# Kernel optimization log

Hardware: AMD Instinct MI355X
Metric: run time of the kernel (lower is better)

The kernel has to match this reference:

```python
import jax, jax.numpy as jnp
import numpy as np
import math

D_MODEL = 256
D_STATE = 16
D_CONV = 4
EXPAND = 2
D_INNER = EXPAND * D_MODEL          # 512
DT_RANK = math.ceil(D_MODEL / 16)   # 16
EPS = 1e-5


def rmsnorm(x, w):
    return x * jax.lax.rsqrt(jnp.mean(x * x, axis=-1, keepdims=True) + EPS) * w


def mamba_mixer(x, in_proj, conv_w, conv_b, x_proj, dt_w, dt_b, A_log, Dp, out_proj):
    # x: [B, L, d_model]
    Bsz, L, _ = x.shape
    xz = x @ in_proj.T                       # [B, L, 2*d_inner]
    xh, z = jnp.split(xz, 2, axis=-1)        # each [B, L, d_inner]
    # causal depthwise conv1d over time (d_conv=4)
    xp = jnp.pad(xh, ((0, 0), (D_CONV - 1, 0), (0, 0)))
    xc = sum(xp[:, k:k + L, :] * conv_w[:, k] for k in range(D_CONV)) + conv_b
    xc = jax.nn.silu(xc)                     # [B, L, d_inner]
    x_dbl = xc @ x_proj.T                    # [B, L, dt_rank + 2*d_state]
    dt, Bm, Cm = jnp.split(x_dbl, [DT_RANK, DT_RANK + D_STATE], axis=-1)
    delta = jax.nn.softplus(dt @ dt_w.T + dt_b)   # [B, L, d_inner]
    A = -jnp.exp(A_log)                      # [d_inner, d_state]
    dA = jnp.exp(jnp.einsum('bld,dn->lbdn', delta, A))        # [L,B,d,n]
    dBu = jnp.einsum('bld,bln,bld->lbdn', delta, Bm, xc)       # [L,B,d,n]

    def step(h, inp):
        a, b = inp
        h = a * h + b
        return h, h

    h0 = jnp.zeros((Bsz, D_INNER, D_STATE), xc.dtype)
    _, hs = jax.lax.scan(step, h0, (dA, dBu))                  # [L,B,d,n]
    y = jnp.einsum('lbdn,bln->bld', hs, Cm) + xc * Dp          # [B,L,d_inner]
    y = y * jax.nn.silu(z)
    return y @ out_proj.T                                      # [B,L,d_model]


def block(x, norm_w, in_proj, conv_w, conv_b, x_proj, dt_w, dt_b, A_log, Dp, out_proj):
    # Block with fused_add_norm=False, residual=None: residual = x, h = mixer(norm(x))
    residual = x
    h = mamba_mixer(rmsnorm(x, norm_w), in_proj, conv_w, conv_b, x_proj,
                    dt_w, dt_b, A_log, Dp, out_proj)
    return h + residual


def setup_inputs() -> dict:
    key = jax.random.key(0)
    ks = jax.random.split(key, 16)
    B, L = 4, 2048

    def n(k, shape, s=0.02):
        return jax.random.normal(k, shape, jnp.float32) * s

    inp = {"x": jax.random.normal(ks[0], (B, L, D_MODEL), jnp.float32)}
    i = 1
    for pre in ("fw", "bw"):
        inp[pre + "_norm"] = jnp.ones((D_MODEL,), jnp.float32)
        inp[pre + "_in_proj"] = n(ks[i], (2 * D_INNER, D_MODEL)); i += 1
        inp[pre + "_conv_w"] = n(ks[i], (D_INNER, D_CONV), 0.1); i += 1
        inp[pre + "_conv_b"] = jnp.zeros((D_INNER,), jnp.float32)
        inp[pre + "_x_proj"] = n(ks[i], (DT_RANK + 2 * D_STATE, D_INNER)); i += 1
        inp[pre + "_dt_w"] = n(ks[i], (D_INNER, DT_RANK), 0.1); i += 1
        inp[pre + "_dt_b"] = n(ks[i], (D_INNER,), 0.1); i += 1
        inp[pre + "_A_log"] = jnp.log(jnp.tile(jnp.arange(1, D_STATE + 1, dtype=jnp.float32), (D_INNER, 1)))
        inp[pre + "_D"] = jnp.ones((D_INNER,), jnp.float32)
        inp[pre + "_out_proj"] = n(ks[i], (D_MODEL, D_INNER)); i += 1
    return inp


def reference(x,
              fw_norm, fw_in_proj, fw_conv_w, fw_conv_b, fw_x_proj, fw_dt_w, fw_dt_b, fw_A_log, fw_D, fw_out_proj,
              bw_norm, bw_in_proj, bw_conv_w, bw_conv_b, bw_x_proj, bw_dt_w, bw_dt_b, bw_A_log, bw_D, bw_out_proj):
    fwd = block(x, fw_norm, fw_in_proj, fw_conv_w, fw_conv_b, fw_x_proj,
                fw_dt_w, fw_dt_b, fw_A_log, fw_D, fw_out_proj)
    xb = jnp.flip(x, axis=1)
    bwd = block(xb, bw_norm, bw_in_proj, bw_conv_w, bw_conv_b, bw_x_proj,
                bw_dt_w, bw_dt_b, bw_A_log, bw_D, bw_out_proj)
    bwd = jnp.flip(bwd, axis=1)
    return fwd + bwd
```

## Files before the change

### kernel.cpp

```cpp
#include <hip/hip_runtime.h>
#include <hip/hip_bf16.h>
#include <math.h>


#define NTOK 8192
#define LL   2048
#define DM   256
#define DI   512
#define DS2  16
#define CL   64
#define NCH  32
#define PLANE 65536
#define KSTEP 64

typedef __bf16 bf16x8 __attribute__((ext_vector_type(8)));
typedef float f32x4 __attribute__((ext_vector_type(4)));

__device__ inline unsigned short f2bf(float f) {
    unsigned u = __float_as_uint(f);
    unsigned r = (u + 0x7fffu + ((u >> 16) & 1u)) >> 16;
    return (unsigned short)r;
}
__device__ inline float bf2f(unsigned short s) {
    return __uint_as_float((unsigned)s << 16);
}

#define L2E 1.4426950408889634f
#define LN2 0.6931471805599453f

__device__ inline float softplus_fast(float x) {
    float e = __builtin_amdgcn_exp2f(-fabsf(x) * L2E);
    float l = __builtin_amdgcn_logf(1.f + e);
    return fmaxf(x, 0.f) + l * LN2;
}

__device__ inline int xcd_swz(int bid, int nwg) {
    int q = nwg >> 3, r = nwg & 7;
    int xcd = bid & 7, lo = bid >> 3;
    return (xcd < r ? xcd * (q + 1) : r * (q + 1) + (xcd - r) * q) + lo;
}

#define GLDS(gp, lp) __builtin_amdgcn_global_load_lds( \
    (const __attribute__((address_space(1))) void*)(gp), \
    (__attribute__((address_space(3))) void*)(lp), 16, 0, 0)

__global__ __launch_bounds__(256) void prep_kernel(
    const float* __restrict__ ip0, const float* __restrict__ nw0,
    const float* __restrict__ ip1, const float* __restrict__ nw1,
    const float* __restrict__ xp0, const float* __restrict__ dtw0,
    const float* __restrict__ xp1, const float* __restrict__ dtw1,
    const float* __restrict__ op0, const float* __restrict__ op1,
    unsigned short* __restrict__ w_in, unsigned short* __restrict__ w_p2,
    unsigned short* __restrict__ w_out,
    const float* __restrict__ x, unsigned short* __restrict__ xn) {
    int bid = blockIdx.x, tid = threadIdx.x;
    if (bid < 2048) {
        int dir = bid >> 10, n = bid & 1023;
        const float* ip = dir ? ip1 : ip0;
        const float* nw = dir ? nw1 : nw0;
        w_in[(size_t)bid * 256 + tid] = f2bf(ip[n * 256 + tid] * nw[tid]);
    } else if (bid < 3200) {
        int idx = bid - 2048;
        int dir = idx / 576, row = idx % 576;
        const float* xp = dir ? xp1 : xp0;
        const float* dtw = dir ? dtw1 : dtw0;
        unsigned short* dst = w_p2 + (size_t)idx * 512;
        for (int k = tid; k < 512; k += 256) {
            float v = 0.f;
            if (row < 512) {
                #pragma unroll
                for (int r = 0; r < 16; ++r) v = fmaf(dtw[row * 16 + r], xp[r * 512 + k], v);
            } else if (row < 544) {
                v = xp[(16 + row - 512) * 512 + k];
            }
            dst[k] = f2bf(v);
        }
    } else if (bid < 3456) {
        int n = bid - 3200;
        for (int k = tid; k < 1024; k += 256) {
            float v = (k < 512) ? op0[n * 512 + k] : op1[n * 512 + (k - 512)];
            w_out[(size_t)n * 1024 + k] = f2bf(v);
        }
    } else {
        int t = bid - 3456;
        float v = x[(size_t)t * DM + tid];
        float ss = v * v;
        #pragma unroll
        for (int m = 1; m < 64; m <<= 1) ss += __shfl_xor(ss, m);
        __shared__ float ws[4];
        if ((tid & 63) == 0) ws[tid >> 6] = ss;
        __syncthreads();
        float tot = ws[0] + ws[1] + ws[2] + ws[3];
        float scale = rsqrtf(tot / (float)DM + 1e-5f);
        xn[(size_t)t * DM + tid] = f2bf(v * scale);
    }
}

#define EPI_IN  0
#define EPI_P2  1
#define EPI_OUT 2

template <int EPI>
__global__ __launch_bounds__(256) void mfma_gemm(
    const unsigned short* __restrict__ A0, const unsigned short* __restrict__ A1,
    const unsigned short* __restrict__ Wb, int K,
    unsigned short* __restrict__ d0, unsigned short* __restrict__ d1,
    unsigned short* __restrict__ e0, unsigned short* __restrict__ e1,
    const float* __restrict__ aux0, const float* __restrict__ aux1,
    const float* __restrict__ Xres, float* __restrict__ outF) {
    __shared__ char lds[2][2][8192];
    int tid = threadIdx.x;
    int lane = tid & 63, wid = tid >> 6;
    int wm = wid >> 1, wn = wid & 1;
    int nwg = gridDim.x * gridDim.y;
    int lid = xcd_swz(blockIdx.y * gridDim.x + blockIdx.x, nwg);
    int n0 = (lid % gridDim.x) * 64;
    int m0 = (lid / gridDim.x) * 64;
    int dir = blockIdx.z;
    const unsigned short* A = dir ? A1 : A0;
    const unsigned short* W = Wb + ((EPI == EPI_P2) ? (size_t)dir * 576 * 512 : 0);

    const int s1 = tid, s2 = tid + 256;
    const int r1 = s1 >> 3, c1 = (s1 & 7) ^ (r1 & 7);
    const int r2 = s2 >> 3, c2 = (s2 & 7) ^ (r2 & 7);

    f32x4 acc[2][2] = {};
    int nt = K / KSTEP;

    auto stage = [&](int t, int buf) {
        int k0 = t * KSTEP;
        GLDS(A + (size_t)(m0 + r1) * K + k0 + c1 * 8, &lds[buf][0][0] + wid * 1024);
        GLDS(A + (size_t)(m0 + r2) * K + k0 + c2 * 8, &lds[buf][0][0] + 4096 + wid * 1024);
        GLDS(W + (size_t)(n0 + r1) * K + k0 + c1 * 8, &lds[buf][1][0] + wid * 1024);
        GLDS(W + (size_t)(n0 + r2) * K + k0 + c2 * 8, &lds[buf][1][0] + 4096 + wid * 1024);
    };

    stage(0, 0);
    for (int t = 0; t < nt; ++t) {
        int buf = t & 1;
        __syncthreads();
        if (t + 1 < nt) stage(t + 1, buf ^ 1);
        const char* Ab = &lds[buf][0][0];
        const char* Bb = &lds[buf][1][0];
        bf16x8 af[2][2], bfv[2][2];
        #pragma unroll
        for (int mf = 0; mf < 2; ++mf)
            #pragma unroll
            for (int kf = 0; kf < 2; ++kf) {
                int r = wm * 32 + mf * 16 + (lane & 15);
                int c = (lane >> 4) + kf * 4;
                af[mf][kf] = *(const bf16x8*)(Ab + r * 128 + ((c ^ (r & 7)) << 4));
            }
        #pragma unroll
        for (int nf = 0; nf < 2; ++nf)
            #pragma unroll
            for (int kf = 0; kf < 2; ++kf) {
                int r = wn * 32 + nf * 16 + (lane & 15);
                int c = (lane >> 4) + kf * 4;
                bfv[nf][kf] = *(const bf16x8*)(Bb + r * 128 + ((c ^ (r & 7)) << 4));
            }
        #pragma unroll
        for (int kf = 0; kf < 2; ++kf)
            #pragma unroll
            for (int mf = 0; mf < 2; ++mf)
                #pragma unroll
                for (int nf = 0; nf < 2; ++nf)
                    acc[mf][nf] = __builtin_amdgcn_mfma_f32_16x16x32_bf16(
                        af[mf][kf], bfv[nf][kf], acc[mf][nf], 0, 0, 0);
    }

    int cb0 = n0 + wn * 32 + (lane & 15);
    int rb0 = m0 + wm * 32 + ((lane >> 4) << 2);
    #pragma unroll
    for (int mf = 0; mf < 2; ++mf)
        #pragma unroll
        for (int nf = 0; nf < 2; ++nf) {
            int n = cb0 + nf * 16;
            #pragma unroll
            for (int r = 0; r < 4; ++r) {
                int m = rb0 + mf * 16 + r;
                float v = acc[mf][nf][r];
                if (EPI == EPI_IN) {
                    d0[(size_t)m * 2048 + n] = f2bf(v);
                } else if (EPI == EPI_P2) {
                    if (n < 512) {
                        float sv = v + (dir ? aux1 : aux0)[n];
                        (dir ? d1 : d0)[(size_t)m * 512 + n] = f2bf(softplus_fast(sv));
                    } else if (n < 544) {
                        (dir ? e1 : e0)[(size_t)m * 32 + (n - 512)] = f2bf(v);
                    }
                } else {
                    outF[(size_t)m * 256 + n] = v + 2.f * Xres[(size_t)m * 256 + n];
                }
            }
        }
}

__global__ __launch_bounds__(256) void conv_silu_kernel(
    const unsigned short* __restrict__ xz,
    const float* __restrict__ cw0, const float* __restrict__ cw1,
    const float* __restrict__ cb0, const float* __restrict__ cb1,
    unsigned short* __restrict__ o0, unsigned short* __restrict__ o1) {
    int dir = blockIdx.y;
    const float* cw = dir ? cw1 : cw0;
    const float* cb = dir ? cb1 : cb0;
    unsigned short* xc = dir ? o1 : o0;
    int idx8 = blockIdx.x * 256 + threadIdx.x;
    int t = idx8 >> 6;
    int c8 = (idx8 & 63) << 3;
    int l = t & (LL - 1);
    const unsigned short* xh = xz + (size_t)dir * 1024 + c8;

    float wreg[32];
    #pragma unroll
    for (int q = 0; q < 8; ++q)
        *(float4*)&wreg[q * 4] = *(const float4*)&cw[c8 * 4 + q * 4];
    float acc[8];
    *(float4*)&acc[0] = *(const float4*)&cb[c8];
    *(float4*)&acc[4] = *(const float4*)&cb[c8 + 4];

    #pragma unroll
    for (int k = 0; k < 4; ++k) {
        int lo = dir ? (l + 3 - k) : (l - 3 + k);
        if (lo < 0 || lo >= LL) continue;
        uint4 u = *(const uint4*)(xh + (size_t)(t + lo - l) * 2048);
        unsigned wv[4] = {u.x, u.y, u.z, u.w};
        #pragma unroll
        for (int j = 0; j < 4; ++j) {
            float flo = __uint_as_float(wv[j] << 16);
            float fhi = __uint_as_float(wv[j] & 0xffff0000u);
            acc[2 * j]     = fmaf(flo, wreg[(2 * j) * 4 + k], acc[2 * j]);
            acc[2 * j + 1] = fmaf(fhi, wreg[(2 * j + 1) * 4 + k], acc[2 * j + 1]);
        }
    }
    unsigned out[4];
    #pragma unroll
    for (int j = 0; j < 4; ++j) {
        float a0 = acc[2 * j], a1 = acc[2 * j + 1];
        float s0 = a0 / (1.f + __expf(-a0));
        float s1 = a1 / (1.f + __expf(-a1));
        out[j] = (unsigned)f2bf(s0) | ((unsigned)f2bf(s1) << 16);
    }
    *(uint4*)(xc + (size_t)idx8 * 8) = make_uint4(out[0], out[1], out[2], out[3]);
}

__global__ __launch_bounds__(256, 4) void scan_part1(
    const unsigned short* __restrict__ dlt0, const unsigned short* __restrict__ dlt1,
    const unsigned short* __restrict__ xc0, const unsigned short* __restrict__ xc1,
    const unsigned short* __restrict__ bc0, const unsigned short* __restrict__ bc1,
    const float* __restrict__ Al0, const float* __restrict__ Al1,
    const float* __restrict__ Dp0, const float* __restrict__ Dp1,
    float* __restrict__ AC, float* __restrict__ HC,
    unsigned* __restrict__ yls0, unsigned* __restrict__ yls1) {
    int dir = blockIdx.z;
    const unsigned short* delta = dir ? dlt1 : dlt0;
    const unsigned short* xc    = dir ? xc1 : xc0;
    const unsigned short* bc    = dir ? bc1 : bc0;
    const float* Alog           = dir ? Al1 : Al0;
    const float* Dp             = dir ? Dp1 : Dp0;
    unsigned* yls               = dir ? yls1 : yls0;
    int b = blockIdx.y >> 5, ch = blockIdx.y & 31;
    int d0 = blockIdx.x * 128;
    int tid = threadIdx.x;
    int dg = tid >> 1, nq = tid & 1;
    int d = d0 + dg;

    __shared__ unsigned sdxu[CL][128];
    __shared__ unsigned sBC[CL][16];
    {
        int row = tid >> 2, q = tid & 3;
        int lr = ch * CL + row;
        int l = dir ? (LL - 1 - lr) : lr;
        size_t t = (size_t)b * LL + l;
        const uint4* dp = (const uint4*)(delta + t * DI + d0 + q * 32);
        const uint4* xp = (const uint4*)(xc + t * DI + d0 + q * 32);
        #pragma unroll
        for (int hh = 0; hh < 4; ++hh) {
            uint4 du = dp[hh], xu = xp[hh];
            unsigned dw[4] = {du.x, du.y, du.z, du.w};
            unsigned xw[4] = {xu.x, xu.y, xu.z, xu.w};
            #pragma unroll
            for (int j = 0; j < 4; ++j) {
                int col = q * 32 + hh * 8 + 2 * j;
                sdxu[row][col ^ row]       = (dw[j] & 0xffffu) | (xw[j] << 16);
                sdxu[row][(col + 1) ^ row] = (dw[j] >> 16) | (xw[j] & 0xffff0000u);
            }
        }
        uint2 Bu = *(const uint2*)(bc + t * 32 + q * 4);
        uint2 Cu = *(const uint2*)(bc + t * 32 + 16 + q * 4);
        sBC[row][q * 4 + 0] = (Bu.x & 0xffffu) | (Cu.x << 16);
        sBC[row][q * 4 + 1] = (Bu.x >> 16) | (Cu.x & 0xffff0000u);
        sBC[row][q * 4 + 2] = (Bu.y & 0xffffu) | (Cu.y << 16);
        sBC[row][q * 4 + 3] = (Bu.y >> 16) | (Cu.y & 0xffff0000u);
    }
    __syncthreads();

    float Av[8], Avl[8];
    {
        float4 Ala = *(const float4*)&Alog[d * DS2 + nq * 8];
        float4 Alb = *(const float4*)&Alog[d * DS2 + nq * 8 + 4];
        Av[0] = -__expf(Ala.x); Av[1] = -__expf(Ala.y);
        Av[2] = -__expf(Ala.z); Av[3] = -__expf(Ala.w);
        Av[4] = -__expf(Alb.x); Av[5] = -__expf(Alb.y);
        Av[6] = -__expf(Alb.z); Av[7] = -__expf(Alb.w);
    }
    #pragma unroll
    for (int j = 0; j < 8; ++j) Avl[j] = Av[j] * L2E;
    bool fast = true;
    #pragma unroll
    for (int j = 0; j < 7; ++j)
        fast = fast && (fabsf(Av[j + 1] - Av[j] + 1.f) < 1e-2f);

    float Dv = Dp[d];
    float h[8] = {0.f, 0.f, 0.f, 0.f, 0.f, 0.f, 0.f, 0.f};
    float sdl = 0.f;
    const float nL2E = -L2E;

    if (fast) {
        #pragma unroll 2
        for (int r = 0; r < CL; ++r) {
            unsigned u = sdxu[r][dg ^ r];
            float dl = __uint_as_float(u << 16);
            float xcv = __uint_as_float(u & 0xffff0000u);
            uint4 q0 = *(const uint4*)&sBC[r][nq * 8];
            uint4 q1 = *(const uint4*)&sBC[r][nq * 8 + 4];
            unsigned bw[8] = {q0.x, q0.y, q0.z, q0.w, q1.x, q1.y, q1.z, q1.w};
            float u0 = dl * xcv;
            sdl += dl;
            float e  = __builtin_amdgcn_exp2f(dl * Avl[0]);
            float rr = __builtin_amdgcn_exp2f(dl * nL2E);
            float ts = 0.f;
            #pragma unroll
            for (int j = 0; j < 8; ++j) {
                float Bf = __uint_as_float(bw[j] << 16);
                float Cf = __uint_as_float(bw[j] & 0xffff0000u);
                h[j] = fmaf(e, h[j], u0 * Bf);
                ts = fmaf(h[j], Cf, ts);
                if (j < 7) e *= rr;
            }
            ts += __shfl_xor(ts, 1);
            if (nq == 0) {
                int lr = ch * CL + r;
                float yv = fmaf(xcv, Dv, ts);
                yls[((size_t)b * LL + lr) * DI + d] =
                    (unsigned)f2bf(yv) | ((unsigned)f2bf(sdl) << 16);
            }
        }
    } else {
        #pragma unroll 2
        for (int r = 0; r < CL; ++r) {
            unsigned u = sdxu[r][dg ^ r];
            float dl = __uint_as_float(u << 16);
            float xcv = __uint_as_float(u & 0xffff0000u);
            uint4 q0 = *(const uint4*)&sBC[r][nq * 8];
            uint4 q1 = *(const uint4*)&sBC[r][nq * 8 + 4];
            unsigned bw[8] = {q0.x, q0.y, q0.z, q0.w, q1.x, q1.y, q1.z, q1.w};
            float u0 = dl * xcv;
            sdl += dl;
            float ts = 0.f;
            #pragma unroll
            for (int j = 0; j < 8; ++j) {
                float Bf = __uint_as_float(bw[j] << 16);
                float Cf = __uint_as_float(bw[j] & 0xffff0000u);
                float e = __builtin_amdgcn_exp2f(dl * Avl[j]);
                h[j] = fmaf(e, h[j], u0 * Bf);
                ts = fmaf(h[j], Cf, ts);
            }
            ts += __shfl_xor(ts, 1);
            if (nq == 0) {
                int lr = ch * CL + r;
                float yv = fmaf(xcv, Dv, ts);
                yls[((size_t)b * LL + lr) * DI + d] =
                    (unsigned)f2bf(yv) | ((unsigned)f2bf(sdl) << 16);
            }
        }
    }

    size_t base = (size_t)ch * PLANE + (size_t)(((dir * 4 + b) * DI + d) * DS2 + nq * 8);
    float ac[8];
    #pragma unroll
    for (int j = 0; j < 8; ++j) ac[j] = __builtin_amdgcn_exp2f(Avl[j] * sdl);
    *(float4*)&AC[base]     = make_float4(ac[0], ac[1], ac[2], ac[3]);
    *(float4*)&AC[base + 4] = make_float4(ac[4], ac[5], ac[6], ac[7]);
    *(float4*)&HC[base]     = make_float4(h[0], h[1], h[2], h[3]);
    *(float4*)&HC[base + 4] = make_float4(h[4], h[5], h[6], h[7]);
}

__global__ __launch_bounds__(256) void scan_part2(
    const float* __restrict__ AC, const float* __restrict__ HC,
    float* __restrict__ HIN) {
    int idx = blockIdx.x * 256 + threadIdx.x;
    float hin = 0.f;
    #pragma unroll
    for (int ch = 0; ch < NCH; ++ch) {
        size_t o = (size_t)ch * PLANE + idx;
        HIN[o] = hin;
        hin = fmaf(AC[o], hin, HC[o]);
    }
}

__global__ __launch_bounds__(256, 8) void scan_lite(
    const unsigned* __restrict__ yls0, const unsigned* __restrict__ yls1,
    const unsigned short* __restrict__ bc0, const unsigned short* __restrict__ bc1,
    const unsigned short* __restrict__ xz,
    const float* __restrict__ Al0, const float* __restrict__ Al1,
    const float* __restrict__ HIN, unsigned short* __restrict__ ycat) {
    int dir = blockIdx.z;
    const unsigned* yls         = dir ? yls1 : yls0;
    const unsigned short* bc    = dir ? bc1 : bc0;
    const float* Alog           = dir ? Al1 : Al0;
    int b = blockIdx.y >> 5, ch = blockIdx.y & 31;
    int d0 = blockIdx.x * 64;
    int tid = threadIdx.x;
    int dg = tid & 63, lg = tid >> 6;
    int d = d0 + dg;

    __shared__ unsigned sC[CL][8];
    {
        int row = tid >> 2, q = tid & 3;
        if (q < 2) {
            int lr = ch * CL + row;
            int l = dir ? (LL - 1 - lr) : lr;
            size_t t = (size_t)b * LL + l;
            uint4 cu = *(const uint4*)(bc + t * 32 + 16 + q * 8);
            *(uint4*)&sC[row][q * 4] = cu;
        }
    }
    __syncthreads();

    float Av[16];
    bool fastA = true;
    #pragma unroll
    for (int qq = 0; qq < 4; ++qq) {
        float4 Al = *(const float4*)&Alog[d * DS2 + qq * 4];
        Av[qq * 4 + 0] = -__expf(Al.x);
        Av[qq * 4 + 1] = -__expf(Al.y);
        Av[qq * 4 + 2] = -__expf(Al.z);
        Av[qq * 4 + 3] = -__expf(Al.w);
    }
    #pragma unroll
    for (int n = 0; n < 16; ++n)
        fastA = fastA && (fabsf(Av[n] + (float)(n + 1)) < 1e-3f * (float)(n + 1));

    float hin[16];
    size_t hbase = (size_t)ch * PLANE + (size_t)(((dir * 4 + b) * DI + d) * DS2);
    #pragma unroll
    for (int qq = 0; qq < 4; ++qq)
        *(float4*)&hin[qq * 4] = *(const float4*)&HIN[hbase + qq * 4];

    #pragma unroll 2
    for (int i = 0; i < 16; ++i) {
        int row = lg * 16 + i;
        int lr = ch * CL + row;
        int ll = dir ? (LL - 1 - lr) : lr;
        size_t tt = (size_t)b * LL + ll;
        unsigned u = yls[((size_t)b * LL + lr) * DI + d];
        float yv = __uint_as_float(u << 16);
        float s  = __uint_as_float(u & 0xffff0000u);
        if (fastA) {
            float E = __builtin_amdgcn_exp2f(-s * L2E);
            if (__any(E > 3e-6f)) {
                float acc = 0.f;
                #pragma unroll
                for (int p = 7; p >= 0; --p) {
                    unsigned cp = sC[row][p];
                    float C0 = __uint_as_float(cp << 16);
                    float C1 = __uint_as_float(cp & 0xffff0000u);
                    acc = fmaf(acc, E, C1 * hin[2 * p + 1]);
                    acc = fmaf(acc, E, C0 * hin[2 * p]);
                }
                yv = fmaf(acc, E, yv);
            }
        } else {
            float acc = 0.f;
            #pragma unroll
            for (int p = 0; p < 8; ++p) {
                unsigned cp = sC[row][p];
                float C0 = __uint_as_float(cp << 16);
                float C1 = __uint_as_float(cp & 0xffff0000u);
                float e0 = __builtin_amdgcn_exp2f(s * Av[2 * p] * L2E);
                float e1 = __builtin_amdgcn_exp2f(s * Av[2 * p + 1] * L2E);
                acc = fmaf(e0 * hin[2 * p], C0, acc);
                acc = fmaf(e1 * hin[2 * p + 1], C1, acc);
            }
            yv += acc;
        }
        float zz = bf2f(xz[tt * 2048 + (size_t)dir * 1024 + 512 + d]);
        yv *= zz / (1.f + __expf(-zz));
        ycat[tt * 1024 + (size_t)dir * 512 + d] = f2bf(yv);
    }
}

extern "C" void kernel_launch(void* const* d_in, const int* in_sizes, int n_in,
                              void* d_out, int out_size, void* d_ws, size_t ws_size,
                              hipStream_t stream) {
    const float* x = (const float*)d_in[0];
    const float* p[2][10];
    for (int dir = 0; dir < 2; ++dir)
        for (int i = 0; i < 10; ++i)
            p[dir][i] = (const float*)d_in[1 + dir * 10 + i];

    char* w = (char*)d_ws;
    auto alloc = [&](size_t bytes) { char* q = w; w += (bytes + 255) & ~(size_t)255; return q; };
    unsigned short* xn    = (unsigned short*)alloc((size_t)NTOK * DM * 2);
    unsigned short* w_in  = (unsigned short*)alloc((size_t)2048 * 256 * 2);
    unsigned short* w_p2  = (unsigned short*)alloc((size_t)1152 * 512 * 2);
    unsigned short* w_out = (unsigned short*)alloc((size_t)256 * 1024 * 2);
    unsigned short* xzcat = (unsigned short*)alloc((size_t)NTOK * 2048 * 2);
    unsigned short *xcb[2], *dlt[2], *bc[2];
    unsigned* yls[2];
    for (int dir = 0; dir < 2; ++dir) {
        xcb[dir] = (unsigned short*)alloc((size_t)NTOK * DI * 2);
        dlt[dir] = (unsigned short*)alloc((size_t)NTOK * DI * 2);
        bc[dir]  = (unsigned short*)alloc((size_t)NTOK * 32 * 2);
        yls[dir] = (unsigned*)alloc((size_t)NTOK * DI * 4);
    }
    unsigned short* ycat = (unsigned short*)alloc((size_t)NTOK * 1024 * 2);
    float* AC  = (float*)alloc((size_t)NCH * PLANE * 4);
    float* HC  = (float*)alloc((size_t)NCH * PLANE * 4);
    float* HIN = (float*)alloc((size_t)NCH * PLANE * 4);
    float* out = (float*)d_out;

    prep_kernel<<<3456 + NTOK, 256, 0, stream>>>(
        p[0][1], p[0][0], p[1][1], p[1][0],
        p[0][4], p[0][5], p[1][4], p[1][5],
        p[0][9], p[1][9], w_in, w_p2, w_out, x, xn);

    mfma_gemm<EPI_IN><<<dim3(32, 128, 1), 256, 0, stream>>>(
        xn, xn, w_in, 256, xzcat, nullptr, nullptr, nullptr,
        nullptr, nullptr, nullptr, nullptr);

    conv_silu_kernel<<<dim3(2048, 2), 256, 0, stream>>>(
        xzcat, p[0][2], p[1][2], p[0][3], p[1][3], xcb[0], xcb[1]);

    mfma_gemm<EPI_P2><<<dim3(9, 128, 2), 256, 0, stream>>>(
        xcb[0], xcb[1], w_p2, 512, dlt[0], dlt[1], bc[0], bc[1],
        p[0][6], p[1][6], nullptr, nullptr);

    scan_part1<<<dim3(DI / 128, 4 * NCH, 2), 256, 0, stream>>>(
        dlt[0], dlt[1], xcb[0], xcb[1], bc[0], bc[1], p[0][7], p[1][7],
        p[0][8], p[1][8], AC, HC, yls[0], yls[1]);
    scan_part2<<<PLANE / 256, 256, 0, stream>>>(AC, HC, HIN);
    scan_lite<<<dim3(DI / 64, 4 * NCH, 2), 256, 0, stream>>>(
        yls[0], yls[1], bc[0], bc[1], xzcat,
        p[0][7], p[1][7], HIN, ycat);

    mfma_gemm<EPI_OUT><<<dim3(4, 128, 1), 256, 0, stream>>>(
        ycat, ycat, w_out, 1024, nullptr, nullptr, nullptr, nullptr,
        nullptr, nullptr, x, out);
}
```

Before: 169.9 us.

## Halve scan_part1 shared staging, transpose yls layout, and break exp dependency chain

scan_part1 now stages the delta/xc chunk in two 32-row halves, which halves the sdxu shared buffer, and raises the launch-bounds occupancy hint from 4 to 8 blocks. The intermediate yls buffer is transposed to a [b][d][l] layout so each thread writes four timesteps in one 16-byte store and scan_part3 reads 16 consecutive values with vector loads. In the fast path, the sequential e*=rr chain is replaced with a power tree, and the C dot product is split into two accumulators to shorten the dependency chains. The cost is an extra pair of barriers, with half the threads idle while each half is staged, and more register pressure under the tighter launch bound.

New measurement: 187.8 us. +10.5%, slower.

```diff
diff --git a/kernel.cpp b/kernel.cpp
--- a/kernel.cpp
+++ b/kernel.cpp
@@ -244,7 +244,7 @@
     *(uint4*)(xc + (size_t)idx8 * 8) = make_uint4(out[0], out[1], out[2], out[3]);
 }
 
-__global__ __launch_bounds__(256, 4) void scan_part1(
+__global__ __launch_bounds__(256, 8) void scan_part1(
     const unsigned short* __restrict__ dlt0, const unsigned short* __restrict__ dlt1,
     const unsigned short* __restrict__ xc0, const unsigned short* __restrict__ xc1,
     const unsigned short* __restrict__ bc0, const unsigned short* __restrict__ bc1,
@@ -265,34 +265,48 @@
     int dg = tid >> 1, nq = tid & 1;
     int d = d0 + dg;
 
-    __shared__ unsigned sdxu[CL][128];
+    __shared__ unsigned sdxu[32][128];
     __shared__ unsigned sBC[CL][16];
-    {
-        int row = tid >> 2, q = tid & 3;
-        int lr = ch * CL + row;
-        int l = dir ? (LL - 1 - lr) : lr;
-        size_t t = (size_t)b * LL + l;
-        const uint4* dp = (const uint4*)(delta + t * DI + d0 + q * 32);
-        const uint4* xp = (const uint4*)(xc + t * DI + d0 + q * 32);
-        #pragma unroll
-        for (int hh = 0; hh < 4; ++hh) {
-            uint4 du = dp[hh], xu = xp[hh];
-            unsigned dw[4] = {du.x, du.y, du.z, du.w};
-            unsigned xw[4] = {xu.x, xu.y, xu.z, xu.w};
-            #pragma unroll
-            for (int j = 0; j < 4; ++j) {
-                int col = q * 32 + hh * 8 + 2 * j;
-                sdxu[row][col ^ row]       = (dw[j] & 0xffffu) | (xw[j] << 16);
-                sdxu[row][(col + 1) ^ row] = (dw[j] >> 16) | (xw[j] & 0xffff0000u);
-            }
-        }
-        uint2 Bu = *(const uint2*)(bc + t * 32 + q * 4);
-        uint2 Cu = *(const uint2*)(bc + t * 32 + 16 + q * 4);
-        sBC[row][q * 4 + 0] = (Bu.x & 0xffffu) | (Cu.x << 16);
-        sBC[row][q * 4 + 1] = (Bu.x >> 16) | (Cu.x & 0xffff0000u);
-        sBC[row][q * 4 + 2] = (Bu.y & 0xffffu) | (Cu.y << 16);
-        sBC[row][q * 4 + 3] = (Bu.y >> 16) | (Cu.y & 0xffff0000u);
-    }
+
+    auto stage_half = [&](int h) {
+        if (tid < 128) {
+            int row = tid >> 2, q = tid & 3;
+            int lr = ch * CL + h * 32 + row;
+            int l = dir ? (LL - 1 - lr) : lr;
+            size_t t = (size_t)b * LL + l;
+            const uint4* dp = (const uint4*)(delta + t * DI + d0);
+            const uint4* xp = (const uint4*)(xc + t * DI + d0);
+            #pragma unroll
+            for (int hh = 0; hh < 4; ++hh) {
+                uint4 du = dp[hh * 4 + q], xu = xp[hh * 4 + q];
+                unsigned dw[4] = {du.x, du.y, du.z, du.w};
+                unsigned xw[4] = {xu.x, xu.y, xu.z, xu.w};
+                #pragma unroll
+                for (int j = 0; j < 4; ++j) {
+                    int col = hh * 32 + q * 8 + 2 * j;
+                    sdxu[row][col ^ row]       = (dw[j] & 0xffffu) | (xw[j] << 16);
+                    sdxu[row][(col + 1) ^ row] = (dw[j] >> 16) | (xw[j] & 0xffff0000u);
+                }
+            }
+        } else if (h == 0) {
+            int tid2 = tid - 128;
+            int row = tid2 >> 1, qh = tid2 & 1;
+            int lr = ch * CL + row;
+            int l = dir ? (LL - 1 - lr) : lr;
+            size_t t = (size_t)b * LL + l;
+            #pragma unroll
+            for (int qi = 0; qi < 2; ++qi) {
+                int q = qh * 2 + qi;
+                uint2 Bu = *(const uint2*)(bc + t * 32 + q * 4);
+                uint2 Cu = *(const uint2*)(bc + t * 32 + 16 + q * 4);
+                *(uint4*)&sBC[row][q * 4] = make_uint4(
+                    (Bu.x & 0xffffu) | (Cu.x << 16), (Bu.x >> 16) | (Cu.x & 0xffff0000u),
+                    (Bu.y & 0xffffu) | (Cu.y << 16), (Bu.y >> 16) | (Cu.y & 0xffff0000u));
+            }
+        }
+    };
+
+    stage_half(0);
     __syncthreads();
 
     float Av[8], Avl[8];
@@ -315,63 +329,79 @@
     float h[8] = {0.f, 0.f, 0.f, 0.f, 0.f, 0.f, 0.f, 0.f};
     float sdl = 0.f;
     const float nL2E = -L2E;
-
-    if (fast) {
-        #pragma unroll 2
-        for (int r = 0; r < CL; ++r) {
-            unsigned u = sdxu[r][dg ^ r];
-            float dl = __uint_as_float(u << 16);
-            float xcv = __uint_as_float(u & 0xffff0000u);
-            uint4 q0 = *(const uint4*)&sBC[r][nq * 8];
-            uint4 q1 = *(const uint4*)&sBC[r][nq * 8 + 4];
-            unsigned bw[8] = {q0.x, q0.y, q0.z, q0.w, q1.x, q1.y, q1.z, q1.w};
-            float u0 = dl * xcv;
-            sdl += dl;
-            float e  = __builtin_amdgcn_exp2f(dl * Avl[0]);
-            float rr = __builtin_amdgcn_exp2f(dl * nL2E);
-            float ts = 0.f;
-            #pragma unroll
-            for (int j = 0; j < 8; ++j) {
-                float Bf = __uint_as_float(bw[j] << 16);
-                float Cf = __uint_as_float(bw[j] & 0xffff0000u);
-                h[j] = fmaf(e, h[j], u0 * Bf);
-                ts = fmaf(h[j], Cf, ts);
-                if (j < 7) e *= rr;
-            }
-            ts += __shfl_xor(ts, 1);
-            if (nq == 0) {
-                int lr = ch * CL + r;
-                float yv = fmaf(xcv, Dv, ts);
-                yls[((size_t)b * LL + lr) * DI + d] =
-                    (unsigned)f2bf(yv) | ((unsigned)f2bf(sdl) << 16);
-            }
-        }
-    } else {
-        #pragma unroll 2
-        for (int r = 0; r < CL; ++r) {
-            unsigned u = sdxu[r][dg ^ r];
-            float dl = __uint_as_float(u << 16);
-            float xcv = __uint_as_float(u & 0xffff0000u);
-            uint4 q0 = *(const uint4*)&sBC[r][nq * 8];
-            uint4 q1 = *(const uint4*)&sBC[r][nq * 8 + 4];
-            unsigned bw[8] = {q0.x, q0.y, q0.z, q0.w, q1.x, q1.y, q1.z, q1.w};
-            float u0 = dl * xcv;
-            sdl += dl;
-            float ts = 0.f;
-            #pragma unroll
-            for (int j = 0; j < 8; ++j) {
-                float Bf = __uint_as_float(bw[j] << 16);
-                float Cf = __uint_as_float(bw[j] & 0xffff0000u);
-                float e = __builtin_amdgcn_exp2f(dl * Avl[j]);
-                h[j] = fmaf(e, h[j], u0 * Bf);
-                ts = fmaf(h[j], Cf, ts);
-            }
-            ts += __shfl_xor(ts, 1);
-            if (nq == 0) {
-                int lr = ch * CL + r;
-                float yv = fmaf(xcv, Dv, ts);
-                yls[((size_t)b * LL + lr) * DI + d] =
-                    (unsigned)f2bf(yv) | ((unsigned)f2bf(sdl) << 16);
+    unsigned ybuf[4];
+    size_t ybase = ((size_t)b * DI + d) * LL + (size_t)ch * CL;
+
+    for (int half = 0; half < 2; ++half) {
+        if (half) { __syncthreads(); stage_half(1); __syncthreads(); }
+        if (fast) {
+            #pragma unroll 2
+            for (int rl = 0; rl < 32; ++rl) {
+                int r = half * 32 + rl;
+                unsigned u = sdxu[rl][dg ^ rl];
+                float dl = __uint_as_float(u << 16);
+                float xcv = __uint_as_float(u & 0xffff0000u);
+                uint4 q0 = *(const uint4*)&sBC[r][nq * 8];
+                uint4 q1 = *(const uint4*)&sBC[r][nq * 8 + 4];
+                unsigned bw[8] = {q0.x, q0.y, q0.z, q0.w, q1.x, q1.y, q1.z, q1.w};
+                float u0 = dl * xcv;
+                sdl += dl;
+                float e0 = __builtin_amdgcn_exp2f(dl * Avl[0]);
+                float rr = __builtin_amdgcn_exp2f(dl * nL2E);
+                float rr2 = rr * rr, rr4 = rr2 * rr2;
+                float e[8];
+                e[0] = e0;         e[1] = e0 * rr;
+                e[2] = e0 * rr2;   e[3] = e[1] * rr2;
+                e[4] = e0 * rr4;   e[5] = e[1] * rr4;
+                e[6] = e[2] * rr4; e[7] = e[3] * rr4;
+                float tsa = 0.f, tsb = 0.f;
+                #pragma unroll
+                for (int j = 0; j < 8; ++j) {
+                    float Bf = __uint_as_float(bw[j] << 16);
+                    float Cf = __uint_as_float(bw[j] & 0xffff0000u);
+                    h[j] = fmaf(e[j], h[j], u0 * Bf);
+                    if (j & 1) tsb = fmaf(h[j], Cf, tsb);
+                    else       tsa = fmaf(h[j], Cf, tsa);
+                }
+                float ts = tsa + tsb;
+                ts += __shfl_xor(ts, 1);
+                if (nq == 0) {
+                    float yv = fmaf(xcv, Dv, ts);
+                    ybuf[r & 3] = (unsigned)f2bf(yv) | ((unsigned)f2bf(sdl) << 16);
+                    if ((r & 3) == 3)
+                        *(uint4*)&yls[ybase + (r - 3)] =
+                            make_uint4(ybuf[0], ybuf[1], ybuf[2], ybuf[3]);
+                }
+            }
+        } else {
+            #pragma unroll 2
+            for (int rl = 0; rl < 32; ++rl) {
+                int r = half * 32 + rl;
+                unsigned u = sdxu[rl][dg ^ rl];
+                float dl = __uint_as_float(u << 16);
+                float xcv = __uint_as_float(u & 0xffff0000u);
+                uint4 q0 = *(const uint4*)&sBC[r][nq * 8];
+                uint4 q1 = *(const uint4*)&sBC[r][nq * 8 + 4];
+                unsigned bw[8] = {q0.x, q0.y, q0.z, q0.w, q1.x, q1.y, q1.z, q1.w};
+                float u0 = dl * xcv;
+                sdl += dl;
+                float ts = 0.f;
+                #pragma unroll
+                for (int j = 0; j < 8; ++j) {
+                    float Bf = __uint_as_float(bw[j] << 16);
+                    float Cf = __uint_as_float(bw[j] & 0xffff0000u);
+                    float e = __builtin_amdgcn_exp2f(dl * Avl[j]);
+                    h[j] = fmaf(e, h[j], u0 * Bf);
+                    ts = fmaf(h[j], Cf, ts);
+                }
+                ts += __shfl_xor(ts, 1);
+                if (nq == 0) {
+                    float yv = fmaf(xcv, Dv, ts);
+                    ybuf[r & 3] = (unsigned)f2bf(yv) | ((unsigned)f2bf(sdl) << 16);
+                    if ((r & 3) == 3)
+                        *(uint4*)&yls[ybase + (r - 3)] =
+                            make_uint4(ybuf[0], ybuf[1], ybuf[2], ybuf[3]);
+                }
             }
         }
     }
@@ -448,13 +478,19 @@
     for (int qq = 0; qq < 4; ++qq)
         *(float4*)&hin[qq * 4] = *(const float4*)&HIN[hbase + qq * 4];
 
+    unsigned yv4[16];
+    const unsigned* yp = &yls[((size_t)b * DI + d) * LL + (size_t)ch * CL + lg * 16];
+    #pragma unroll
+    for (int k = 0; k < 4; ++k)
+        *(uint4*)&yv4[k * 4] = *(const uint4*)(yp + k * 4);
+
     #pragma unroll 2
     for (int i = 0; i < 16; ++i) {
         int row = lg * 16 + i;
         int lr = ch * CL + row;
         int ll = dir ? (LL - 1 - lr) : lr;
         size_t tt = (size_t)b * LL + ll;
-        unsigned u = yls[((size_t)b * LL + lr) * DI + d];
+        unsigned u = yv4[i];
         float yv = __uint_as_float(u << 16);
         float s  = __uint_as_float(u & 0xffff0000u);
         if (fastA) {
```

## Halve scan chunk length, double chunk count, and shorten per-step decay chain

Applied to the files above, without the earlier changes.

Cuts the chunked selective-scan chunk length from 64 to 32 and doubles the chunk count, remapping the shared-memory staging loads in scan_part1 and scan_lite and raising scan_part1's occupancy hint to 8. This gives more concurrent blocks and a shorter serial recurrence per block. Inside the fast path, the per-state decay factors are now computed as a shallow tree of powers instead of a serial multiply chain, and the C-dot product uses two accumulators to add instruction-level parallelism. The cost is more chunk-boundary state traffic through AC/HC/HIN and a longer serial loop in scan_part2.

Result: no change. 171.4 us (+0.9%).

```diff
diff --git a/kernel.cpp b/kernel.cpp
--- a/kernel.cpp
+++ b/kernel.cpp
@@ -8,8 +8,8 @@
 #define DM   256
 #define DI   512
 #define DS2  16
-#define CL   64
-#define NCH  32
+#define CL   32
+#define NCH  64
 #define PLANE 65536
 #define KSTEP 64
 
@@ -244,7 +244,7 @@
     *(uint4*)(xc + (size_t)idx8 * 8) = make_uint4(out[0], out[1], out[2], out[3]);
 }
 
-__global__ __launch_bounds__(256, 4) void scan_part1(
+__global__ __launch_bounds__(256, 8) void scan_part1(
     const unsigned short* __restrict__ dlt0, const unsigned short* __restrict__ dlt1,
     const unsigned short* __restrict__ xc0, const unsigned short* __restrict__ xc1,
     const unsigned short* __restrict__ bc0, const unsigned short* __restrict__ bc1,
@@ -259,7 +259,7 @@
     const float* Alog           = dir ? Al1 : Al0;
     const float* Dp             = dir ? Dp1 : Dp0;
     unsigned* yls               = dir ? yls1 : yls0;
-    int b = blockIdx.y >> 5, ch = blockIdx.y & 31;
+    int b = blockIdx.y >> 6, ch = blockIdx.y & 63;
     int d0 = blockIdx.x * 128;
     int tid = threadIdx.x;
     int dg = tid >> 1, nq = tid & 1;
@@ -268,30 +268,31 @@
     __shared__ unsigned sdxu[CL][128];
     __shared__ unsigned sBC[CL][16];
     {
-        int row = tid >> 2, q = tid & 3;
+        int row = tid >> 3, q = tid & 7;
         int lr = ch * CL + row;
         int l = dir ? (LL - 1 - lr) : lr;
         size_t t = (size_t)b * LL + l;
-        const uint4* dp = (const uint4*)(delta + t * DI + d0 + q * 32);
-        const uint4* xp = (const uint4*)(xc + t * DI + d0 + q * 32);
-        #pragma unroll
-        for (int hh = 0; hh < 4; ++hh) {
-            uint4 du = dp[hh], xu = xp[hh];
+        const uint4* dp = (const uint4*)(delta + t * DI + d0);
+        const uint4* xp = (const uint4*)(xc + t * DI + d0);
+        #pragma unroll
+        for (int hh = 0; hh < 2; ++hh) {
+            uint4 du = dp[q * 2 + hh], xu = xp[q * 2 + hh];
             unsigned dw[4] = {du.x, du.y, du.z, du.w};
             unsigned xw[4] = {xu.x, xu.y, xu.z, xu.w};
             #pragma unroll
             for (int j = 0; j < 4; ++j) {
-                int col = q * 32 + hh * 8 + 2 * j;
+                int col = q * 16 + hh * 8 + 2 * j;
                 sdxu[row][col ^ row]       = (dw[j] & 0xffffu) | (xw[j] << 16);
                 sdxu[row][(col + 1) ^ row] = (dw[j] >> 16) | (xw[j] & 0xffff0000u);
             }
         }
-        uint2 Bu = *(const uint2*)(bc + t * 32 + q * 4);
-        uint2 Cu = *(const uint2*)(bc + t * 32 + 16 + q * 4);
-        sBC[row][q * 4 + 0] = (Bu.x & 0xffffu) | (Cu.x << 16);
-        sBC[row][q * 4 + 1] = (Bu.x >> 16) | (Cu.x & 0xffff0000u);
-        sBC[row][q * 4 + 2] = (Bu.y & 0xffffu) | (Cu.y << 16);
-        sBC[row][q * 4 + 3] = (Bu.y >> 16) | (Cu.y & 0xffff0000u);
+        if (q < 4) {
+            uint2 Bu = *(const uint2*)(bc + t * 32 + q * 4);
+            uint2 Cu = *(const uint2*)(bc + t * 32 + 16 + q * 4);
+            *(uint4*)&sBC[row][q * 4] = make_uint4(
+                (Bu.x & 0xffffu) | (Cu.x << 16), (Bu.x >> 16) | (Cu.x & 0xffff0000u),
+                (Bu.y & 0xffffu) | (Cu.y << 16), (Bu.y >> 16) | (Cu.y & 0xffff0000u));
+        }
     }
     __syncthreads();
 
@@ -327,17 +328,24 @@
             unsigned bw[8] = {q0.x, q0.y, q0.z, q0.w, q1.x, q1.y, q1.z, q1.w};
             float u0 = dl * xcv;
             sdl += dl;
-            float e  = __builtin_amdgcn_exp2f(dl * Avl[0]);
+            float e0 = __builtin_amdgcn_exp2f(dl * Avl[0]);
             float rr = __builtin_amdgcn_exp2f(dl * nL2E);
-            float ts = 0.f;
+            float rr2 = rr * rr, rr4 = rr2 * rr2;
+            float e[8];
+            e[0] = e0;         e[1] = e0 * rr;
+            e[2] = e0 * rr2;   e[3] = e[1] * rr2;
+            e[4] = e0 * rr4;   e[5] = e[1] * rr4;
+            e[6] = e[2] * rr4; e[7] = e[3] * rr4;
+            float tsa = 0.f, tsb = 0.f;
             #pragma unroll
             for (int j = 0; j < 8; ++j) {
                 float Bf = __uint_as_float(bw[j] << 16);
                 float Cf = __uint_as_float(bw[j] & 0xffff0000u);
-                h[j] = fmaf(e, h[j], u0 * Bf);
-                ts = fmaf(h[j], Cf, ts);
-                if (j < 7) e *= rr;
-            }
+                h[j] = fmaf(e[j], h[j], u0 * Bf);
+                if (j & 1) tsb = fmaf(h[j], Cf, tsb);
+                else       tsa = fmaf(h[j], Cf, tsa);
+            }
+            float ts = tsa + tsb;
             ts += __shfl_xor(ts, 1);
             if (nq == 0) {
                 int lr = ch * CL + r;
@@ -391,7 +399,7 @@
     float* __restrict__ HIN) {
     int idx = blockIdx.x * 256 + threadIdx.x;
     float hin = 0.f;
-    #pragma unroll
+    #pragma unroll 8
     for (int ch = 0; ch < NCH; ++ch) {
         size_t o = (size_t)ch * PLANE + idx;
         HIN[o] = hin;
@@ -409,22 +417,20 @@
     const unsigned* yls         = dir ? yls1 : yls0;
     const unsigned short* bc    = dir ? bc1 : bc0;
     const float* Alog           = dir ? Al1 : Al0;
-    int b = blockIdx.y >> 5, ch = blockIdx.y & 31;
+    int b = blockIdx.y >> 6, ch = blockIdx.y & 63;
     int d0 = blockIdx.x * 64;
     int tid = threadIdx.x;
     int dg = tid & 63, lg = tid >> 6;
     int d = d0 + dg;
 
     __shared__ unsigned sC[CL][8];
-    {
-        int row = tid >> 2, q = tid & 3;
-        if (q < 2) {
-            int lr = ch * CL + row;
-            int l = dir ? (LL - 1 - lr) : lr;
-            size_t t = (size_t)b * LL + l;
-            uint4 cu = *(const uint4*)(bc + t * 32 + 16 + q * 8);
-            *(uint4*)&sC[row][q * 4] = cu;
-        }
+    if (tid < 64) {
+        int row = tid >> 1, q = tid & 1;
+        int lr = ch * CL + row;
+        int l = dir ? (LL - 1 - lr) : lr;
+        size_t t = (size_t)b * LL + l;
+        uint4 cu = *(const uint4*)(bc + t * 32 + 16 + q * 8);
+        *(uint4*)&sC[row][q * 4] = cu;
     }
     __syncthreads();
 
@@ -449,8 +455,8 @@
         *(float4*)&hin[qq * 4] = *(const float4*)&HIN[hbase + qq * 4];
 
     #pragma unroll 2
-    for (int i = 0; i < 16; ++i) {
-        int row = lg * 16 + i;
+    for (int i = 0; i < 8; ++i) {
+        int row = lg * 8 + i;
         int lr = ch * CL + row;
         int ll = dir ? (LL - 1 - lr) : lr;
         size_t tt = (size_t)b * LL + ll;
```

## Assign one channel per thread with all 16 states in scan_part1

Applied to the files above, without the earlier changes.

scan_part1 now runs 128 threads per block, each owning a single d channel and all 16 state entries, where before two threads split the 16 states and combined results with a shuffle. B and C are stored in shared memory already converted to float, the decay powers come from a power-of-two tree instead of a serial multiply chain, and the C dot product uses four partial accumulators. This removes the cross-lane shuffle and halves the redundant delta/x work per channel, at the cost of more registers per thread and half as many threads per block, which lowers occupancy and latency hiding.

Result: no change. 168.6 us (-0.8%).

```diff
diff --git a/kernel.cpp b/kernel.cpp
--- a/kernel.cpp
+++ b/kernel.cpp
@@ -244,7 +244,7 @@
     *(uint4*)(xc + (size_t)idx8 * 8) = make_uint4(out[0], out[1], out[2], out[3]);
 }
 
-__global__ __launch_bounds__(256, 4) void scan_part1(
+__global__ __launch_bounds__(128, 2) void scan_part1(
     const unsigned short* __restrict__ dlt0, const unsigned short* __restrict__ dlt1,
     const unsigned short* __restrict__ xc0, const unsigned short* __restrict__ xc1,
     const unsigned short* __restrict__ bc0, const unsigned short* __restrict__ bc1,
@@ -262,128 +262,138 @@
     int b = blockIdx.y >> 5, ch = blockIdx.y & 31;
     int d0 = blockIdx.x * 128;
     int tid = threadIdx.x;
-    int dg = tid >> 1, nq = tid & 1;
-    int d = d0 + dg;
+    int d = d0 + tid;
 
     __shared__ unsigned sdxu[CL][128];
-    __shared__ unsigned sBC[CL][16];
+    __shared__ float sB[CL][16];
+    __shared__ float sC[CL][16];
     {
-        int row = tid >> 2, q = tid & 3;
+        int row = tid >> 1, q2 = tid & 1;
         int lr = ch * CL + row;
         int l = dir ? (LL - 1 - lr) : lr;
         size_t t = (size_t)b * LL + l;
-        const uint4* dp = (const uint4*)(delta + t * DI + d0 + q * 32);
-        const uint4* xp = (const uint4*)(xc + t * DI + d0 + q * 32);
-        #pragma unroll
-        for (int hh = 0; hh < 4; ++hh) {
+        const uint4* dp = (const uint4*)(delta + t * DI + d0) + q2 * 8;
+        const uint4* xp = (const uint4*)(xc + t * DI + d0) + q2 * 8;
+        #pragma unroll
+        for (int hh = 0; hh < 8; ++hh) {
             uint4 du = dp[hh], xu = xp[hh];
             unsigned dw[4] = {du.x, du.y, du.z, du.w};
             unsigned xw[4] = {xu.x, xu.y, xu.z, xu.w};
             #pragma unroll
             for (int j = 0; j < 4; ++j) {
-                int col = q * 32 + hh * 8 + 2 * j;
+                int col = q2 * 64 + hh * 8 + 2 * j;
                 sdxu[row][col ^ row]       = (dw[j] & 0xffffu) | (xw[j] << 16);
                 sdxu[row][(col + 1) ^ row] = (dw[j] >> 16) | (xw[j] & 0xffff0000u);
             }
         }
-        uint2 Bu = *(const uint2*)(bc + t * 32 + q * 4);
-        uint2 Cu = *(const uint2*)(bc + t * 32 + 16 + q * 4);
-        sBC[row][q * 4 + 0] = (Bu.x & 0xffffu) | (Cu.x << 16);
-        sBC[row][q * 4 + 1] = (Bu.x >> 16) | (Cu.x & 0xffff0000u);
-        sBC[row][q * 4 + 2] = (Bu.y & 0xffffu) | (Cu.y << 16);
-        sBC[row][q * 4 + 3] = (Bu.y >> 16) | (Cu.y & 0xffff0000u);
+        uint4 Bu = *(const uint4*)(bc + t * 32 + q2 * 8);
+        uint4 Cu = *(const uint4*)(bc + t * 32 + 16 + q2 * 8);
+        unsigned bw[4] = {Bu.x, Bu.y, Bu.z, Bu.w};
+        unsigned cw[4] = {Cu.x, Cu.y, Cu.z, Cu.w};
+        #pragma unroll
+        for (int j = 0; j < 4; ++j) {
+            sB[row][q2 * 8 + 2 * j]     = __uint_as_float(bw[j] << 16);
+            sB[row][q2 * 8 + 2 * j + 1] = __uint_as_float(bw[j] & 0xffff0000u);
+            sC[row][q2 * 8 + 2 * j]     = __uint_as_float(cw[j] << 16);
+            sC[row][q2 * 8 + 2 * j + 1] = __uint_as_float(cw[j] & 0xffff0000u);
+        }
     }
     __syncthreads();
 
-    float Av[8], Avl[8];
-    {
-        float4 Ala = *(const float4*)&Alog[d * DS2 + nq * 8];
-        float4 Alb = *(const float4*)&Alog[d * DS2 + nq * 8 + 4];
-        Av[0] = -__expf(Ala.x); Av[1] = -__expf(Ala.y);
-        Av[2] = -__expf(Ala.z); Av[3] = -__expf(Ala.w);
-        Av[4] = -__expf(Alb.x); Av[5] = -__expf(Alb.y);
-        Av[6] = -__expf(Alb.z); Av[7] = -__expf(Alb.w);
-    }
-    #pragma unroll
-    for (int j = 0; j < 8; ++j) Avl[j] = Av[j] * L2E;
+    float Av[16], Avl[16];
+    #pragma unroll
+    for (int qq = 0; qq < 4; ++qq) {
+        float4 Al = *(const float4*)&Alog[d * DS2 + qq * 4];
+        Av[qq * 4 + 0] = -__expf(Al.x);
+        Av[qq * 4 + 1] = -__expf(Al.y);
+        Av[qq * 4 + 2] = -__expf(Al.z);
+        Av[qq * 4 + 3] = -__expf(Al.w);
+    }
+    #pragma unroll
+    for (int j = 0; j < 16; ++j) Avl[j] = Av[j] * L2E;
     bool fast = true;
     #pragma unroll
-    for (int j = 0; j < 7; ++j)
+    for (int j = 0; j < 15; ++j)
         fast = fast && (fabsf(Av[j + 1] - Av[j] + 1.f) < 1e-2f);
 
     float Dv = Dp[d];
-    float h[8] = {0.f, 0.f, 0.f, 0.f, 0.f, 0.f, 0.f, 0.f};
+    float h[16];
+    #pragma unroll
+    for (int j = 0; j < 16; ++j) h[j] = 0.f;
     float sdl = 0.f;
     const float nL2E = -L2E;
 
     if (fast) {
-        #pragma unroll 2
         for (int r = 0; r < CL; ++r) {
-            unsigned u = sdxu[r][dg ^ r];
+            unsigned u = sdxu[r][tid ^ r];
             float dl = __uint_as_float(u << 16);
             float xcv = __uint_as_float(u & 0xffff0000u);
-            uint4 q0 = *(const uint4*)&sBC[r][nq * 8];
-            uint4 q1 = *(const uint4*)&sBC[r][nq * 8 + 4];
-            unsigned bw[8] = {q0.x, q0.y, q0.z, q0.w, q1.x, q1.y, q1.z, q1.w};
+            float Bv[16], Cv[16];
+            #pragma unroll
+            for (int k = 0; k < 4; ++k) {
+                *(float4*)&Bv[k * 4] = *(const float4*)&sB[r][k * 4];
+                *(float4*)&Cv[k * 4] = *(const float4*)&sC[r][k * 4];
+            }
             float u0 = dl * xcv;
             sdl += dl;
-            float e  = __builtin_amdgcn_exp2f(dl * Avl[0]);
+            float e0 = __builtin_amdgcn_exp2f(dl * Avl[0]);
             float rr = __builtin_amdgcn_exp2f(dl * nL2E);
-            float ts = 0.f;
-            #pragma unroll
-            for (int j = 0; j < 8; ++j) {
-                float Bf = __uint_as_float(bw[j] << 16);
-                float Cf = __uint_as_float(bw[j] & 0xffff0000u);
-                h[j] = fmaf(e, h[j], u0 * Bf);
-                ts = fmaf(h[j], Cf, ts);
-                if (j < 7) e *= rr;
-            }
-            ts += __shfl_xor(ts, 1);
-            if (nq == 0) {
-                int lr = ch * CL + r;
-                float yv = fmaf(xcv, Dv, ts);
-                yls[((size_t)b * LL + lr) * DI + d] =
-                    (unsigned)f2bf(yv) | ((unsigned)f2bf(sdl) << 16);
-            }
+            float rr2 = rr * rr, rr4 = rr2 * rr2, rr8 = rr4 * rr4;
+            float e[16];
+            e[0] = e0;       e[1] = e0 * rr;
+            e[2] = e0 * rr2; e[3] = e[1] * rr2;
+            #pragma unroll
+            for (int j = 0; j < 4; ++j) e[4 + j] = e[j] * rr4;
+            #pragma unroll
+            for (int j = 0; j < 8; ++j) e[8 + j] = e[j] * rr8;
+            float t0 = 0.f, t1 = 0.f, t2 = 0.f, t3 = 0.f;
+            #pragma unroll
+            for (int j = 0; j < 4; ++j) {
+                h[4*j+0] = fmaf(e[4*j+0], h[4*j+0], u0 * Bv[4*j+0]);
+                h[4*j+1] = fmaf(e[4*j+1], h[4*j+1], u0 * Bv[4*j+1]);
+                h[4*j+2] = fmaf(e[4*j+2], h[4*j+2], u0 * Bv[4*j+2]);
+                h[4*j+3] = fmaf(e[4*j+3], h[4*j+3], u0 * Bv[4*j+3]);
+                t0 = fmaf(h[4*j+0], Cv[4*j+0], t0);
+                t1 = fmaf(h[4*j+1], Cv[4*j+1], t1);
+                t2 = fmaf(h[4*j+2], Cv[4*j+2], t2);
+                t3 = fmaf(h[4*j+3], Cv[4*j+3], t3);
+            }
+            float ts = (t0 + t1) + (t2 + t3);
+            int lr = ch * CL + r;
+            float yv = fmaf(xcv, Dv, ts);
+            yls[((size_t)b * LL + lr) * DI + d] =
+                (unsigned)f2bf(yv) | ((unsigned)f2bf(sdl) << 16);
         }
     } else {
-        #pragma unroll 2
         for (int r = 0; r < CL; ++r) {
-            unsigned u = sdxu[r][dg ^ r];
+            unsigned u = sdxu[r][tid ^ r];
             float dl = __uint_as_float(u << 16);
             float xcv = __uint_as_float(u & 0xffff0000u);
-            uint4 q0 = *(const uint4*)&sBC[r][nq * 8];
-            uint4 q1 = *(const uint4*)&sBC[r][nq * 8 + 4];
-            unsigned bw[8] = {q0.x, q0.y, q0.z, q0.w, q1.x, q1.y, q1.z, q1.w};
             float u0 = dl * xcv;
             sdl += dl;
             float ts = 0.f;
             #pragma unroll
-            for (int j = 0; j < 8; ++j) {
-                float Bf = __uint_as_float(bw[j] << 16);
-                float Cf = __uint_as_float(bw[j] & 0xffff0000u);
+            for (int j = 0; j < 16; ++j) {
                 float e = __builtin_amdgcn_exp2f(dl * Avl[j]);
-                h[j] = fmaf(e, h[j], u0 * Bf);
-                ts = fmaf(h[j], Cf, ts);
-            }
-            ts += __shfl_xor(ts, 1);
-            if (nq == 0) {
-                int lr = ch * CL + r;
-                float yv = fmaf(xcv, Dv, ts);
-                yls[((size_t)b * LL + lr) * DI + d] =
-                    (unsigned)f2bf(yv) | ((unsigned)f2bf(sdl) << 16);
-            }
-        }
-    }
-
-    size_t base = (size_t)ch * PLANE + (size_t)(((dir * 4 + b) * DI + d) * DS2 + nq * 8);
-    float ac[8];
-    #pragma unroll
-    for (int j = 0; j < 8; ++j) ac[j] = __builtin_amdgcn_exp2f(Avl[j] * sdl);
-    *(float4*)&AC[base]     = make_float4(ac[0], ac[1], ac[2], ac[3]);
-    *(float4*)&AC[base + 4] = make_float4(ac[4], ac[5], ac[6], ac[7]);
-    *(float4*)&HC[base]     = make_float4(h[0], h[1], h[2], h[3]);
-    *(float4*)&HC[base + 4] = make_float4(h[4], h[5], h[6], h[7]);
+                h[j] = fmaf(e, h[j], u0 * sB[r][j]);
+                ts = fmaf(h[j], sC[r][j], ts);
+            }
+            int lr = ch * CL + r;
+            float yv = fmaf(xcv, Dv, ts);
+            yls[((size_t)b * LL + lr) * DI + d] =
+                (unsigned)f2bf(yv) | ((unsigned)f2bf(sdl) << 16);
+        }
+    }
+
+    size_t base = (size_t)ch * PLANE + (size_t)(((dir * 4 + b) * DI + d) * DS2);
+    float ac[16];
+    #pragma unroll
+    for (int j = 0; j < 16; ++j) ac[j] = __builtin_amdgcn_exp2f(Avl[j] * sdl);
+    #pragma unroll
+    for (int k = 0; k < 4; ++k) {
+        *(float4*)&AC[base + k * 4] = *(const float4*)&ac[k * 4];
+        *(float4*)&HC[base + k * 4] = *(const float4*)&h[k * 4];
+    }
 }
 
 __global__ __launch_bounds__(256) void scan_part2(
@@ -537,7 +547,7 @@
         xcb[0], xcb[1], w_p2, 512, dlt[0], dlt[1], bc[0], bc[1],
         p[0][6], p[1][6], nullptr, nullptr);
 
-    scan_part1<<<dim3(DI / 128, 4 * NCH, 2), 256, 0, stream>>>(
+    scan_part1<<<dim3(DI / 128, 4 * NCH, 2), 128, 0, stream>>>(
         dlt[0], dlt[1], xcb[0], xcb[1], bc[0], bc[1], p[0][7], p[1][7],
         p[0][8], p[1][8], AC, HC, yls[0], yls[1]);
     scan_part2<<<PLANE / 256, 256, 0, stream>>>(AC, HC, HIN);
```
